# Kernel tuning notes

Measured on AMD Instinct MI355X. Metric: run time of the kernel, lower is better.

## Reference

```python
import jax, jax.numpy as jnp
import numpy as np
import math

N_HEADS = 16
D_HEAD = 128
D_ROPE = 32
SPLIT = D_HEAD - D_ROPE  # 96
LATENT = 512
D_MODEL = 2048
B, T = 2, 2048


def _rotary_emb(num_tokens, d_rope):
    inv_freq = 1.0 / (10000.0 ** (jnp.arange(0, d_rope, 2, dtype=jnp.float32) / d_rope))
    t = jnp.arange(num_tokens, dtype=jnp.float32)
    freqs = jnp.einsum('t,f->tf', t, inv_freq)          # [T, d_rope/2]
    return jnp.concatenate([freqs, freqs], axis=-1)      # [T, d_rope]


def _apply_rotary(x, cos, sin):
    # x: [B,T,H,d_rope]; cos/sin: [1,T,1,d_rope]
    half = x.shape[-1] // 2
    x1, x2 = x[..., :half], x[..., half:]
    rot = jnp.concatenate([-x2, x1], axis=-1)
    return x * cos + rot * sin


def setup_inputs() -> dict:
    key = jax.random.key(0)
    ks = jax.random.split(key, 20)
    s = 0.02
    def w(k, i, o):
        return jax.random.normal(k, (i, o), dtype=jnp.float32) * s
    inp = {
        'input': jax.random.normal(ks[0], (B, T, D_MODEL), dtype=jnp.float32),
        'batch_size': B,
        'num_tokens': T,
        'Wdkv_w': w(ks[1], D_MODEL, LATENT), 'Wdkv_b': jnp.zeros((LATENT,), jnp.float32),
        'Wdq_w':  w(ks[2], D_MODEL, LATENT), 'Wdq_b':  jnp.zeros((LATENT,), jnp.float32),
        'Wuk_w':  w(ks[3], LATENT, N_HEADS * SPLIT),  'Wuk_b': jnp.zeros((N_HEADS * SPLIT,), jnp.float32),
        'Wuv_w':  w(ks[4], LATENT, N_HEADS * D_HEAD), 'Wuv_b': jnp.zeros((N_HEADS * D_HEAD,), jnp.float32),
        'Wuq_w':  w(ks[5], LATENT, N_HEADS * SPLIT),  'Wuq_b': jnp.zeros((N_HEADS * SPLIT,), jnp.float32),
        'Wqr_w':  w(ks[6], LATENT, N_HEADS * D_ROPE), 'Wqr_b': jnp.zeros((N_HEADS * D_ROPE,), jnp.float32),
        'Wkr_w':  w(ks[7], D_MODEL, N_HEADS * D_ROPE), 'Wkr_b': jnp.zeros((N_HEADS * D_ROPE,), jnp.float32),
        'Wo_w':   w(ks[8], N_HEADS * D_HEAD, D_MODEL), 'Wo_b': jnp.zeros((D_MODEL,), jnp.float32),
    }
    return inp


def reference(input, batch_size, num_tokens,
              Wdkv_w, Wdkv_b, Wdq_w, Wdq_b, Wuk_w, Wuk_b, Wuv_w, Wuv_b,
              Wuq_w, Wuq_b, Wqr_w, Wqr_b, Wkr_w, Wkr_b, Wo_w, Wo_b):
    lin = lambda x, w, b: x @ w + b
    bsz, T_ = batch_size, num_tokens

    c_kv = lin(input, Wdkv_w, Wdkv_b)                                   # [B,T,latent]
    k_base = lin(c_kv, Wuk_w, Wuk_b).reshape(bsz, T_, N_HEADS, SPLIT)
    v = lin(c_kv, Wuv_w, Wuv_b).reshape(bsz, T_, N_HEADS, D_HEAD)

    c_q = lin(input, Wdq_w, Wdq_b)
    q_base = lin(c_q, Wuq_w, Wuq_b).reshape(bsz, T_, N_HEADS, SPLIT)
    q_rot = lin(c_q, Wqr_w, Wqr_b).reshape(bsz, T_, N_HEADS, D_ROPE)

    emb = _rotary_emb(T_, D_ROPE)                                        # [T,d_rope]
    cos = jnp.cos(emb)[None, :, None, :]
    sin = jnp.sin(emb)[None, :, None, :]
    q_rot = _apply_rotary(q_rot, cos, sin)
    k_rot = _apply_rotary(lin(input, Wkr_w, Wkr_b).reshape(bsz, T_, N_HEADS, D_ROPE), cos, sin)

    q = jnp.concatenate([q_base, q_rot], axis=-1)                        # [B,T,H,d_head]
    k = jnp.concatenate([k_base, k_rot], axis=-1)

    scores = jnp.einsum('bqhd,bkhd->bhqk', q, k) / math.sqrt(D_HEAD)
    attn = jax.nn.softmax(scores, axis=-1)
    out = jnp.einsum('bhqk,bkhd->bqhd', attn, v)
    out = lin(out.reshape(bsz, T_, N_HEADS * D_HEAD), Wo_w, Wo_b)
    return out, c_kv, k_rot
```

## Files before the change

kernel.cpp:

```cpp
#include <hip/hip_runtime.h>

typedef __bf16 bf16x8 __attribute__((ext_vector_type(8)));
typedef float f32x4 __attribute__((ext_vector_type(4)));
typedef float f32x16 __attribute__((ext_vector_type(16)));

#define NROWS 4096
#define DM 2048
#define LAT 512
#define NH 16
#define DH 128

__device__ __forceinline__ unsigned short f2bf(float f) {
    union { float f; unsigned u; } v; v.f = f;
    unsigned r = v.u + 0x7fffu + ((v.u >> 16) & 1u);
    return (unsigned short)(r >> 16);
}
__device__ __forceinline__ void gload16(const void* g, void* l) {
    __builtin_amdgcn_global_load_lds((const __attribute__((address_space(1))) unsigned int*)g,
                                     (__attribute__((address_space(3))) unsigned int*)l, 16, 0, 0);
}
__device__ __forceinline__ unsigned cvtpk_bf16(float lo, float hi) {
    unsigned r;
    asm("v_cvt_pk_bf16_f32 %0, %1, %2" : "=v"(r) : "v"(lo), "v"(hi));
    return r;
}
__device__ __forceinline__ void pl32swap(unsigned& a, unsigned& b) {
    asm("v_permlane32_swap_b32 %0, %1" : "+v"(a), "+v"(b));
}
__device__ __forceinline__ float exp2a(float x) {
    float r;
    asm("v_exp_f32 %0, %1" : "=v"(r) : "v"(x));
    return r;
}

struct PrepParams {
    const float* tsrc[8]; unsigned short* tdst[8];
    int tK[8]; int tN[8]; int tstart[8];
    const float* input; unsigned short* xbf;
    float* cs; float* sn;
    const float* bsrc[8]; float* bdst[8]; int blen[8];
};

#define PREP_T_END   9984
#define PREP_X_END   18176
#define PREP_R_END   18304
#define PREP_B_END   18340

__global__ __launch_bounds__(256) void prep_kernel(PrepParams P) {
    const int bid = blockIdx.x, tid = threadIdx.x;
    if (bid < PREP_T_END) {
        int j = 0;
        #pragma unroll
        for (int i = 1; i < 8; ++i) if (bid >= P.tstart[i]) j = i;
        const int local = bid - P.tstart[j];
        const float* W = P.tsrc[j];
        unsigned short* Wt = P.tdst[j];
        const int K = P.tK[j], N = P.tN[j];
        const int nbx = N >> 5;
        const int nb = (local % nbx) * 32, kb = (local / nbx) * 32;
        __shared__ float tile[32][33];
        const int tx = tid & 31, ty = tid >> 5;
        #pragma unroll
        for (int i = 0; i < 32; i += 8)
            tile[ty + i][tx] = W[(size_t)(kb + ty + i) * N + nb + tx];
        __syncthreads();
        #pragma unroll
        for (int i = 0; i < 32; i += 8)
            Wt[(size_t)(nb + ty + i) * K + kb + tx] = f2bf(tile[tx][ty + i]);
    } else if (bid < PREP_X_END) {
        const int i = ((bid - PREP_T_END) * 256 + tid) * 4;
        float4 v = *(const float4*)(P.input + i);
        unsigned short* y = P.xbf + i;
        y[0] = f2bf(v.x); y[1] = f2bf(v.y); y[2] = f2bf(v.z); y[3] = f2bf(v.w);
    } else if (bid < PREP_R_END) {
        const int idx = (bid - PREP_X_END) * 256 + tid;
        const int i = idx & 15, t = idx >> 4;
        float inv = powf(10000.0f, -(float)i / 16.0f);
        float a = (float)t * inv;
        P.cs[idx] = cosf(a);
        P.sn[idx] = sinf(a);
    } else {
        const int gid = (bid - PREP_R_END) * 256 + tid;
        int off = 0;
        #pragma unroll
        for (int i = 0; i < 8; ++i) {
            if (gid >= off && gid < off + P.blen[i])
                P.bdst[i][gid - off] = P.bsrc[i][gid - off];
            off += P.blen[i];
        }
    }
}

__global__ __launch_bounds__(256) void gemm_fused_kernel(const unsigned short* __restrict__ A,
                                                         const unsigned short* __restrict__ Bt,
                                                         const float* __restrict__ biascat,
                                                         int K, int which,
                                                         float* __restrict__ outF,
                                                         unsigned short* __restrict__ outB0,
                                                         unsigned short* __restrict__ outB1,
                                                         unsigned short* __restrict__ outB0k,
                                                         float* __restrict__ outRope,
                                                         const float* __restrict__ cs,
                                                         const float* __restrict__ sn) {
    __shared__ __align__(16) unsigned short SM[2][8192];
    const int tid = threadIdx.x;
    const int mb = blockIdx.x * 128;
    const int by = blockIdx.y, nb = by * 128;
    const int w = tid >> 6, lane = tid & 63;
    const int wr = (w >> 1) * 64, wc = (w & 1) * 64;
    const int l15 = lane & 15, l4 = lane >> 4;
    const int srow = lane >> 2, sko = (lane & 3) * 8;

    f32x4 acc[4][4] = {};

    auto STAGE = [&](int buf, int k0) {
        #pragma unroll
        for (int c = 0; c < 16; c += 4) {
            int cc = c + w;
            if (cc < 8)
                gload16(A + (size_t)(mb + cc * 16 + srow) * K + k0 + sko, SM[buf] + cc * 512);
            else
                gload16(Bt + (size_t)(nb + (cc - 8) * 16 + srow) * K + k0 + sko, SM[buf] + 4096 + (cc - 8) * 512);
        }
    };

    const int nk = K >> 5;
    STAGE(0, 0);
    for (int kt = 0; kt < nk; ++kt) {
        const int buf = kt & 1;
        if (kt + 1 < nk) {
            STAGE(buf ^ 1, (kt + 1) << 5);
            asm volatile("s_waitcnt vmcnt(4)" ::: "memory");
        } else {
            asm volatile("s_waitcnt vmcnt(0)" ::: "memory");
        }
        __builtin_amdgcn_sched_barrier(0);
        __builtin_amdgcn_s_barrier();
        __builtin_amdgcn_sched_barrier(0);

        const unsigned short* As = SM[buf];
        const unsigned short* Bs = SM[buf] + 4096;
        bf16x8 af[4], bfr[4];
        #pragma unroll
        for (int mi = 0; mi < 4; ++mi)
            af[mi] = *(const bf16x8*)(As + (wr + mi * 16 + l15) * 32 + l4 * 8);
        #pragma unroll
        for (int ni = 0; ni < 4; ++ni)
            bfr[ni] = *(const bf16x8*)(Bs + (wc + ni * 16 + l15) * 32 + l4 * 8);
        #pragma unroll
        for (int mi = 0; mi < 4; ++mi)
            #pragma unroll
            for (int ni = 0; ni < 4; ++ni)
                acc[mi][ni] = __builtin_amdgcn_mfma_f32_16x16x32_bf16(af[mi], bfr[ni], acc[mi][ni], 0, 0, 0);
        __builtin_amdgcn_s_barrier();
    }

    if (which == 1 && by >= 12) {
        unsigned short* BT = &SM[0][0];
        const int c2b = nb - 1536;
        #pragma unroll
        for (int half = 0; half < 2; ++half) {
            __syncthreads();
            if ((wr >> 6) == half) {
                #pragma unroll
                for (int mi = 0; mi < 4; ++mi)
                    #pragma unroll
                    for (int ni = 0; ni < 4; ++ni) {
                        const int col = wc + ni * 16 + l15;
                        const float bv = biascat[nb + col];
                        ushort4 pv;
                        pv.x = f2bf(acc[mi][ni][0] + bv);
                        pv.y = f2bf(acc[mi][ni][1] + bv);
                        pv.z = f2bf(acc[mi][ni][2] + bv);
                        pv.w = f2bf(acc[mi][ni][3] + bv);
                        *(ushort4*)(BT + col * 72 + mi * 16 + l4 * 4) = pv;
                    }
            }
            __syncthreads();
            const int c = tid >> 1;
            #pragma unroll
            for (int j = 0; j < 4; ++j) {
                const int seg = (tid & 1) * 4 + j;
                uint4 val = *(const uint4*)(BT + c * 72 + seg * 8);
                *(uint4*)(outB1 + (size_t)(c2b + c) * 4096 + mb + half * 64 + seg * 8) = val;
            }
        }
        return;
    }

    #pragma unroll
    for (int mi = 0; mi < 4; ++mi) {
        const int row0 = mb + wr + mi * 16 + l4 * 4;
        #pragma unroll
        for (int ni = 0; ni < 4; ++ni) {
            const int colg = nb + wc + ni * 16 + l15;
            const float bv = biascat[colg];
            float v[4];
            #pragma unroll
            for (int r = 0; r < 4; ++r) v[r] = acc[mi][ni][r] + bv;

            if (which == 0) {
                if (by < 4) {
                    #pragma unroll
                    for (int r = 0; r < 4; ++r) {
                        outF[(size_t)(row0 + r) * 512 + colg] = v[r];
                        outB0[(size_t)(row0 + r) * 512 + colg] = f2bf(v[r]);
                    }
                } else if (by < 8) {
                    const int c2 = colg - 512;
                    #pragma unroll
                    for (int r = 0; r < 4; ++r)
                        outB1[(size_t)(row0 + r) * 512 + c2] = f2bf(v[r]);
                } else {
                    const int cloc = colg - 1024, i2 = cloc & 31, h2 = cloc >> 5;
                    const float pbv = biascat[colg ^ 16];
                    const bool lo = (ni & 1) == 0;
                    #pragma unroll
                    for (int r = 0; r < 4; ++r) {
                        float vp = acc[mi][ni ^ 1][r] + pbv;
                        int t = (row0 + r) & 2047;
                        float cc_ = cs[t * 16 + (i2 & 15)], ss_ = sn[t * 16 + (i2 & 15)];
                        float o = lo ? (v[r] * cc_ - vp * ss_) : (v[r] * cc_ + vp * ss_);
                        outRope[(size_t)(row0 + r) * 512 + cloc] = o;
                        outB0k[(size_t)(row0 + r) * 2048 + h2 * 128 + 96 + i2] = f2bf(o);
                    }
                }
            } else if (which == 1) {
                const int ocol = (colg / 96) * 128 + colg % 96;
                #pragma unroll
                for (int r = 0; r < 4; ++r)
                    outB0[(size_t)(row0 + r) * 2048 + ocol] = f2bf(v[r]);
            } else if (which == 2) {
                if (by < 12) {
                    const int ocol = (colg / 96) * 128 + colg % 96;
                    #pragma unroll
                    for (int r = 0; r < 4; ++r)
                        outB0[(size_t)(row0 + r) * 2048 + ocol] = f2bf(v[r]);
                } else {
                    const int cloc = colg - 1536, i2 = cloc & 31, h2 = cloc >> 5;
                    const float pbv = biascat[colg ^ 16];
                    const bool lo = (ni & 1) == 0;
                    #pragma unroll
                    for (int r = 0; r < 4; ++r) {
                        float vp = acc[mi][ni ^ 1][r] + pbv;
                        int t = (row0 + r) & 2047;
                        float cc_ = cs[t * 16 + (i2 & 15)], ss_ = sn[t * 16 + (i2 & 15)];
                        float o = lo ? (v[r] * cc_ - vp * ss_) : (v[r] * cc_ + vp * ss_);
                        outB0[(size_t)(row0 + r) * 2048 + h2 * 128 + 96 + i2] = f2bf(o);
                    }
                }
            } else {
                #pragma unroll
                for (int r = 0; r < 4; ++r)
                    outF[(size_t)(row0 + r) * 2048 + colg] = v[r];
            }
        }
    }
}

__global__ __launch_bounds__(256, 2) void attn_kernel(const unsigned short* __restrict__ Q,
                                                      const unsigned short* __restrict__ Kb,
                                                      const unsigned short* __restrict__ Vtg,
                                                      unsigned short* __restrict__ O) {
    __shared__ __align__(16) unsigned short Ks[2][64 * 128];
    __shared__ __align__(16) unsigned short Vs[2][128 * 64];

    const int tid = threadIdx.x, w = tid >> 6, lane = tid & 63;
    const int l31 = lane & 31, hi = lane >> 5;
    const int bid = blockIdx.x;
    const int logical = (bid & 7) * 64 + (bid >> 3);
    const int bh = logical >> 4, b = bh >> 4, h = bh & 15;
    const int qt = (logical & 15) * 128 + w * 32;
    const int qrow = qt + l31;
    const float sl2e = 0.08838834764831845f * 1.4426950408889634f;

    bf16x8 qf[8];
    const unsigned short* qptr = Q + (size_t)(b * 2048 + qrow) * 2048 + h * 128 + hi * 8;
    #pragma unroll
    for (int s = 0; s < 8; ++s) qf[s] = *(const bf16x8*)(qptr + s * 16);

    f32x16 acc[4] = {};
    float m_run = -1e30f, l_run = 0.0f;

    const int kl15 = lane >> 4, kd0 = lane & 15;
    const int vr = lane >> 3, vk = lane & 7;

    auto STAGE = [&](int buf, int kt) {
        #pragma unroll
        for (int i = 0; i < 4; ++i) {
            int c = w * 4 + i;
            int key = c * 4 + kl15;
            int d0 = (kd0 * 8) ^ ((key & 7) << 3);
            gload16(Kb + (size_t)(b * 2048 + kt + key) * 2048 + h * 128 + d0, &Ks[buf][c * 512]);
            int dv = c * 8 + vr;
            int k0 = (vk * 8) ^ ((dv & 7) << 3);
            gload16(Vtg + (size_t)(h * 128 + dv) * 4096 + b * 2048 + kt + k0, &Vs[buf][c * 512]);
        }
    };

    STAGE(0, 0);

    for (int t = 0; t < 32; ++t) {
        const int buf = t & 1;
        if (t < 31) {
            STAGE(buf ^ 1, (t + 1) * 64);
            asm volatile("s_waitcnt vmcnt(8)" ::: "memory");
        } else {
            asm volatile("s_waitcnt vmcnt(0)" ::: "memory");
        }
        __builtin_amdgcn_sched_barrier(0);
        __builtin_amdgcn_s_barrier();
        __builtin_amdgcn_sched_barrier(0);

        #pragma unroll
        for (int g = 0; g < 2; ++g) {
            const int key = g * 32 + l31;
            const unsigned short* kbase = &Ks[buf][key * 128];
            const int ksw = (key & 7) << 3;
            f32x16 sc = {};
            __builtin_amdgcn_s_setprio(1);
            #pragma unroll
            for (int s = 0; s < 8; ++s) {
                bf16x8 kf = *(const bf16x8*)(kbase + ((s * 16 + hi * 8) ^ ksw));
                sc = __builtin_amdgcn_mfma_f32_32x32x16_bf16(kf, qf[s], sc, 0, 0, 0);
            }
            __builtin_amdgcn_s_setprio(0);

            float pm = sc[0];
            #pragma unroll
            for (int i = 1; i < 16; ++i) pm = fmaxf(pm, sc[i]);
            pm = fmaxf(pm, __shfl_xor(pm, 32, 64));

            if (__any(pm > m_run + 90.51f)) {
                float mn = fmaxf(m_run, pm);
                float f = exp2a((m_run - mn) * sl2e);
                m_run = mn;
                l_run *= f;
                #pragma unroll
                for (int dg = 0; dg < 4; ++dg)
                    #pragma unroll
                    for (int i = 0; i < 16; ++i) acc[dg][i] *= f;
            }
            const float mexp2 = m_run * sl2e;

            float rs = 0.0f;
            #pragma unroll
            for (int s2 = 0; s2 < 2; ++s2) {
                float e[8];
                #pragma unroll
                for (int j = 0; j < 8; ++j) {
                    e[j] = exp2a(fmaf(sc[s2 * 8 + j], sl2e, -mexp2));
                    rs += e[j];
                }
                unsigned X0 = cvtpk_bf16(e[0], e[1]), X1 = cvtpk_bf16(e[2], e[3]);
                unsigned Y0 = cvtpk_bf16(e[4], e[5]), Y1 = cvtpk_bf16(e[6], e[7]);
                pl32swap(X0, Y0);
                pl32swap(X1, Y1);
                union { unsigned u[4]; bf16x8 v; } pf;
                pf.u[0] = X0; pf.u[1] = X1; pf.u[2] = Y0; pf.u[3] = Y1;

                const int kofs = g * 32 + s2 * 16 + hi * 8;
                __builtin_amdgcn_s_setprio(1);
                #pragma unroll
                for (int dg = 0; dg < 4; ++dg) {
                    const int d = dg * 32 + l31;
                    bf16x8 vf = *(const bf16x8*)(&Vs[buf][d * 64 + (kofs ^ ((d & 7) << 3))]);
                    acc[dg] = __builtin_amdgcn_mfma_f32_32x32x16_bf16(vf, pf.v, acc[dg], 0, 0, 0);
                }
                __builtin_amdgcn_s_setprio(0);
            }
            rs += __shfl_xor(rs, 32, 64);
            l_run += rs;
        }
        __builtin_amdgcn_s_barrier();
    }

    const float inv = 1.0f / l_run;
    unsigned short* obase = O + (size_t)(b * 2048 + qrow) * 2048 + h * 128;
    #pragma unroll
    for (int dg = 0; dg < 4; ++dg)
        #pragma unroll
        for (int k = 0; k < 4; ++k) {
            ushort4 pv;
            pv.x = f2bf(acc[dg][4 * k + 0] * inv);
            pv.y = f2bf(acc[dg][4 * k + 1] * inv);
            pv.z = f2bf(acc[dg][4 * k + 2] * inv);
            pv.w = f2bf(acc[dg][4 * k + 3] * inv);
            *(ushort4*)(obase + dg * 32 + k * 8 + hi * 4) = pv;
        }
}

extern "C" void kernel_launch(void* const* d_in, const int* in_sizes, int n_in,
                              void* d_out, int out_size, void* d_ws, size_t ws_size,
                              hipStream_t stream) {
    (void)in_sizes; (void)n_in; (void)out_size; (void)ws_size;

    const float* input  = (const float*)d_in[0];
    const float* Wdkv_w = (const float*)d_in[3];
    const float* Wdkv_b = (const float*)d_in[4];
    const float* Wdq_w  = (const float*)d_in[5];
    const float* Wdq_b  = (const float*)d_in[6];
    const float* Wuk_w  = (const float*)d_in[7];
    const float* Wuk_b  = (const float*)d_in[8];
    const float* Wuv_w  = (const float*)d_in[9];
    const float* Wuv_b  = (const float*)d_in[10];
    const float* Wuq_w  = (const float*)d_in[11];
    const float* Wuq_b  = (const float*)d_in[12];
    const float* Wqr_w  = (const float*)d_in[13];
    const float* Wqr_b  = (const float*)d_in[14];
    const float* Wkr_w  = (const float*)d_in[15];
    const float* Wkr_b  = (const float*)d_in[16];
    const float* Wo_w   = (const float*)d_in[17];
    const float* Wo_b   = (const float*)d_in[18];

    float* out_main = (float*)d_out;
    float* out_ckv  = out_main + (size_t)NROWS * DM;
    float* out_krot = out_ckv + (size_t)NROWS * LAT;

    char* p = (char*)d_ws;
    auto alloc = [&](size_t bytes) { char* r = p; p += (bytes + 255) & ~(size_t)255; return r; };
    unsigned short* x_bf  = (unsigned short*)alloc((size_t)NROWS * DM * 2);
    unsigned short* w1_t  = (unsigned short*)alloc((size_t)1536 * DM * 2);
    unsigned short* w2_t  = (unsigned short*)alloc((size_t)3584 * LAT * 2);
    unsigned short* w3_t  = (unsigned short*)alloc((size_t)2048 * LAT * 2);
    unsigned short* w4_t  = (unsigned short*)alloc((size_t)DM * DM * 2);
    unsigned short* ckv_bf = (unsigned short*)alloc((size_t)NROWS * LAT * 2);
    unsigned short* cq_bf  = (unsigned short*)alloc((size_t)NROWS * LAT * 2);
    unsigned short* q_bf   = (unsigned short*)alloc((size_t)NROWS * DM * 2);
    unsigned short* k_bf   = (unsigned short*)alloc((size_t)NROWS * DM * 2);
    unsigned short* vt_g   = (unsigned short*)alloc((size_t)DM * NROWS * 2);
    unsigned short* ao_bf  = (unsigned short*)alloc((size_t)NROWS * DM * 2);
    float* cos_t = (float*)alloc((size_t)2048 * 16 * 4);
    float* sin_t = (float*)alloc((size_t)2048 * 16 * 4);
    float* bc1 = (float*)alloc(1536 * 4);
    float* bc2 = (float*)alloc(3584 * 4);
    float* bc3 = (float*)alloc(2048 * 4);
    float* bc4 = (float*)alloc(2048 * 4);

    PrepParams P;
    const float* tsrc[8] = {Wdkv_w, Wdq_w, Wkr_w, Wuk_w, Wuv_w, Wuq_w, Wqr_w, Wo_w};
    unsigned short* tdst[8] = {w1_t, w1_t + 512 * 2048, w1_t + 1024 * 2048,
                               w2_t, w2_t + 1536 * 512, w3_t, w3_t + 1536 * 512, w4_t};
    int tK[8] = {2048, 2048, 2048, 512, 512, 512, 512, 2048};
    int tN[8] = {512, 512, 512, 1536, 2048, 1536, 512, 2048};
    int tstart[8] = {0, 1024, 2048, 3072, 3840, 4864, 5632, 5888};
    const float* bsrc[8] = {Wdkv_b, Wdq_b, Wkr_b, Wuk_b, Wuv_b, Wuq_b, Wqr_b, Wo_b};
    float* bdst[8] = {bc1, bc1 + 512, bc1 + 1024, bc2, bc2 + 1536, bc3, bc3 + 1536, bc4};
    int blen[8] = {512, 512, 512, 1536, 2048, 1536, 512, 2048};
    for (int i = 0; i < 8; ++i) {
        P.tsrc[i] = tsrc[i]; P.tdst[i] = tdst[i]; P.tK[i] = tK[i]; P.tN[i] = tN[i];
        P.tstart[i] = tstart[i]; P.bsrc[i] = bsrc[i]; P.bdst[i] = bdst[i]; P.blen[i] = blen[i];
    }
    P.input = input; P.xbf = x_bf; P.cs = cos_t; P.sn = sin_t;
    prep_kernel<<<PREP_B_END, 256, 0, stream>>>(P);

    gemm_fused_kernel<<<dim3(32, 12), 256, 0, stream>>>(x_bf, w1_t, bc1, 2048, 0,
                                                        out_ckv, ckv_bf, cq_bf, k_bf, out_krot, cos_t, sin_t);
    gemm_fused_kernel<<<dim3(32, 28), 256, 0, stream>>>(ckv_bf, w2_t, bc2, 512, 1,
                                                        nullptr, k_bf, vt_g, nullptr, nullptr, nullptr, nullptr);
    gemm_fused_kernel<<<dim3(32, 16), 256, 0, stream>>>(cq_bf, w3_t, bc3, 512, 2,
                                                        nullptr, q_bf, nullptr, nullptr, nullptr, cos_t, sin_t);

    attn_kernel<<<512, 256, 0, stream>>>(q_bf, k_bf, vt_g, ao_bf);

    gemm_fused_kernel<<<dim3(32, 16), 256, 0, stream>>>(ao_bf, w4_t, bc4, 2048, 3,
                                                        out_main, nullptr, nullptr, nullptr, nullptr, nullptr, nullptr);
}
```

Before: 239.0 us.

## Split attention over two key halves with merge kernel and single-buffered V

Splits each attention block's key range into two halves, so the grid doubles to 1024 blocks. Each block writes unnormalized bf16 partial outputs plus running max and sum, and a new merge kernel combines them. V staging drops to a single buffer that loads while QK/softmax runs, QK MFMAs are split into two independent accumulator chains, and launch bounds rise to 3 blocks per CU. This targets low occupancy and serialized MFMA dependencies in the original 512-block launch. In exchange it adds partial-output traffic, an extra launch, and extra rounding from storing unnormalized partials in bf16.

```diff
diff --git a/kernel.cpp b/kernel.cpp
--- a/kernel.cpp
+++ b/kernel.cpp
@@ -258,20 +258,23 @@
     }
 }
 
-__global__ __launch_bounds__(256, 2) void attn_kernel(const unsigned short* __restrict__ Q,
+__global__ __launch_bounds__(256, 3) void attn_kernel(const unsigned short* __restrict__ Q,
                                                       const unsigned short* __restrict__ Kb,
                                                       const unsigned short* __restrict__ Vtg,
-                                                      unsigned short* __restrict__ O) {
+                                                      unsigned short* __restrict__ p0,
+                                                      unsigned short* __restrict__ p1,
+                                                      float* __restrict__ pml) {
     __shared__ __align__(16) unsigned short Ks[2][64 * 128];
-    __shared__ __align__(16) unsigned short Vs[2][128 * 64];
+    __shared__ __align__(16) unsigned short Vs[128 * 64];
 
     const int tid = threadIdx.x, w = tid >> 6, lane = tid & 63;
     const int l31 = lane & 31, hi = lane >> 5;
     const int bid = blockIdx.x;
-    const int logical = (bid & 7) * 64 + (bid >> 3);
-    const int bh = logical >> 4, b = bh >> 4, h = bh & 15;
-    const int qt = (logical & 15) * 128 + w * 32;
-    const int qrow = qt + l31;
+    const int logical = (bid & 7) * 128 + (bid >> 3);
+    const int bh = logical >> 5, b = bh >> 4, h = bh & 15;
+    const int ks = (logical >> 4) & 1;
+    const int qrow = (logical & 15) * 128 + w * 32 + l31;
+    const int kbase = ks * 1024;
     const float sl2e = 0.08838834764831845f * 1.4426950408889634f;
 
     bf16x8 qf[8];
@@ -285,50 +288,60 @@
     const int kl15 = lane >> 4, kd0 = lane & 15;
     const int vr = lane >> 3, vk = lane & 7;
 
-    auto STAGE = [&](int buf, int kt) {
+    auto STAGE_K = [&](int buf, int kt) {
         #pragma unroll
         for (int i = 0; i < 4; ++i) {
             int c = w * 4 + i;
             int key = c * 4 + kl15;
             int d0 = (kd0 * 8) ^ ((key & 7) << 3);
             gload16(Kb + (size_t)(b * 2048 + kt + key) * 2048 + h * 128 + d0, &Ks[buf][c * 512]);
+        }
+    };
+    auto STAGE_V = [&](int kt) {
+        #pragma unroll
+        for (int i = 0; i < 4; ++i) {
+            int c = w * 4 + i;
             int dv = c * 8 + vr;
             int k0 = (vk * 8) ^ ((dv & 7) << 3);
-            gload16(Vtg + (size_t)(h * 128 + dv) * 4096 + b * 2048 + kt + k0, &Vs[buf][c * 512]);
+            gload16(Vtg + (size_t)(h * 128 + dv) * 4096 + b * 2048 + kt + k0, &Vs[c * 512]);
         }
     };
 
-    STAGE(0, 0);
-
-    for (int t = 0; t < 32; ++t) {
+    STAGE_K(0, kbase);
+    asm volatile("s_waitcnt vmcnt(0)" ::: "memory");
+    __builtin_amdgcn_sched_barrier(0);
+    __builtin_amdgcn_s_barrier();
+    __builtin_amdgcn_sched_barrier(0);
+
+    for (int t = 0; t < 16; ++t) {
         const int buf = t & 1;
-        if (t < 31) {
-            STAGE(buf ^ 1, (t + 1) * 64);
-            asm volatile("s_waitcnt vmcnt(8)" ::: "memory");
-        } else {
-            asm volatile("s_waitcnt vmcnt(0)" ::: "memory");
-        }
-        __builtin_amdgcn_sched_barrier(0);
-        __builtin_amdgcn_s_barrier();
-        __builtin_amdgcn_sched_barrier(0);
-
+        STAGE_V(kbase + t * 64);
+        if (t < 15) STAGE_K(buf ^ 1, kbase + (t + 1) * 64);
+
+        unsigned pfu[2][2][4];
         #pragma unroll
         for (int g = 0; g < 2; ++g) {
             const int key = g * 32 + l31;
-            const unsigned short* kbase = &Ks[buf][key * 128];
+            const unsigned short* kbse = &Ks[buf][key * 128];
             const int ksw = (key & 7) << 3;
-            f32x16 sc = {};
+            f32x16 scA = {}, scB = {};
             __builtin_amdgcn_s_setprio(1);
             #pragma unroll
-            for (int s = 0; s < 8; ++s) {
-                bf16x8 kf = *(const bf16x8*)(kbase + ((s * 16 + hi * 8) ^ ksw));
-                sc = __builtin_amdgcn_mfma_f32_32x32x16_bf16(kf, qf[s], sc, 0, 0, 0);
+            for (int s = 0; s < 4; ++s) {
+                bf16x8 kfA = *(const bf16x8*)(kbse + ((s * 16 + hi * 8) ^ ksw));
+                bf16x8 kfB = *(const bf16x8*)(kbse + (((s + 4) * 16 + hi * 8) ^ ksw));
+                scA = __builtin_amdgcn_mfma_f32_32x32x16_bf16(kfA, qf[s], scA, 0, 0, 0);
+                scB = __builtin_amdgcn_mfma_f32_32x32x16_bf16(kfB, qf[s + 4], scB, 0, 0, 0);
             }
             __builtin_amdgcn_s_setprio(0);
-
-            float pm = sc[0];
-            #pragma unroll
-            for (int i = 1; i < 16; ++i) pm = fmaxf(pm, sc[i]);
+            f32x16 sc = scA + scB;
+
+            float t0 = fmaxf(sc[0], sc[1]),  t1 = fmaxf(sc[2], sc[3]);
+            float t2 = fmaxf(sc[4], sc[5]),  t3 = fmaxf(sc[6], sc[7]);
+            float t4 = fmaxf(sc[8], sc[9]),  t5 = fmaxf(sc[10], sc[11]);
+            float t6 = fmaxf(sc[12], sc[13]), t7 = fmaxf(sc[14], sc[15]);
+            float pm = fmaxf(fmaxf(fmaxf(t0, t1), fmaxf(t2, t3)),
+                             fmaxf(fmaxf(t4, t5), fmaxf(t6, t7)));
             pm = fmaxf(pm, __shfl_xor(pm, 32, 64));
 
             if (__any(pm > m_run + 90.51f)) {
@@ -343,51 +356,107 @@
             }
             const float mexp2 = m_run * sl2e;
 
-            float rs = 0.0f;
+            float e[16];
+            #pragma unroll
+            for (int j = 0; j < 16; ++j)
+                e[j] = exp2a(fmaf(sc[j], sl2e, -mexp2));
+            float a0 = e[0] + e[1], a1 = e[2] + e[3], a2 = e[4] + e[5], a3 = e[6] + e[7];
+            float a4 = e[8] + e[9], a5 = e[10] + e[11], a6 = e[12] + e[13], a7 = e[14] + e[15];
+            l_run += ((a0 + a1) + (a2 + a3)) + ((a4 + a5) + (a6 + a7));
+
             #pragma unroll
             for (int s2 = 0; s2 < 2; ++s2) {
-                float e[8];
-                #pragma unroll
-                for (int j = 0; j < 8; ++j) {
-                    e[j] = exp2a(fmaf(sc[s2 * 8 + j], sl2e, -mexp2));
-                    rs += e[j];
-                }
-                unsigned X0 = cvtpk_bf16(e[0], e[1]), X1 = cvtpk_bf16(e[2], e[3]);
-                unsigned Y0 = cvtpk_bf16(e[4], e[5]), Y1 = cvtpk_bf16(e[6], e[7]);
+                unsigned X0 = cvtpk_bf16(e[s2 * 8 + 0], e[s2 * 8 + 1]);
+                unsigned X1 = cvtpk_bf16(e[s2 * 8 + 2], e[s2 * 8 + 3]);
+                unsigned Y0 = cvtpk_bf16(e[s2 * 8 + 4], e[s2 * 8 + 5]);
+                unsigned Y1 = cvtpk_bf16(e[s2 * 8 + 6], e[s2 * 8 + 7]);
                 pl32swap(X0, Y0);
                 pl32swap(X1, Y1);
+                pfu[g][s2][0] = X0; pfu[g][s2][1] = X1;
+                pfu[g][s2][2] = Y0; pfu[g][s2][3] = Y1;
+            }
+        }
+
+        if (t < 15) asm volatile("s_waitcnt vmcnt(4)" ::: "memory");
+        else        asm volatile("s_waitcnt vmcnt(0)" ::: "memory");
+        __builtin_amdgcn_sched_barrier(0);
+        __builtin_amdgcn_s_barrier();
+        __builtin_amdgcn_sched_barrier(0);
+
+        __builtin_amdgcn_s_setprio(1);
+        #pragma unroll
+        for (int g = 0; g < 2; ++g)
+            #pragma unroll
+            for (int s2 = 0; s2 < 2; ++s2) {
                 union { unsigned u[4]; bf16x8 v; } pf;
-                pf.u[0] = X0; pf.u[1] = X1; pf.u[2] = Y0; pf.u[3] = Y1;
-
+                pf.u[0] = pfu[g][s2][0]; pf.u[1] = pfu[g][s2][1];
+                pf.u[2] = pfu[g][s2][2]; pf.u[3] = pfu[g][s2][3];
                 const int kofs = g * 32 + s2 * 16 + hi * 8;
-                __builtin_amdgcn_s_setprio(1);
                 #pragma unroll
                 for (int dg = 0; dg < 4; ++dg) {
                     const int d = dg * 32 + l31;
-                    bf16x8 vf = *(const bf16x8*)(&Vs[buf][d * 64 + (kofs ^ ((d & 7) << 3))]);
+                    bf16x8 vf = *(const bf16x8*)(&Vs[d * 64 + (kofs ^ ((d & 7) << 3))]);
                     acc[dg] = __builtin_amdgcn_mfma_f32_32x32x16_bf16(vf, pf.v, acc[dg], 0, 0, 0);
                 }
-                __builtin_amdgcn_s_setprio(0);
-            }
-            rs += __shfl_xor(rs, 32, 64);
-            l_run += rs;
-        }
-        __builtin_amdgcn_s_barrier();
-    }
-
-    const float inv = 1.0f / l_run;
-    unsigned short* obase = O + (size_t)(b * 2048 + qrow) * 2048 + h * 128;
+            }
+        __builtin_amdgcn_s_setprio(0);
+
+        if (t < 15) {
+            asm volatile("s_waitcnt vmcnt(0)" ::: "memory");
+            __builtin_amdgcn_sched_barrier(0);
+            __builtin_amdgcn_s_barrier();
+            __builtin_amdgcn_sched_barrier(0);
+        }
+    }
+
+    l_run += __shfl_xor(l_run, 32, 64);
+    unsigned short* pOut = (ks ? p1 : p0) + (size_t)(bh * 2048 + qrow) * 128;
+    if (hi == 0) {
+        float2 ml; ml.x = m_run; ml.y = l_run;
+        *(float2*)(pml + ((size_t)(ks * 32 + bh) * 2048 + qrow) * 2) = ml;
+    }
     #pragma unroll
     for (int dg = 0; dg < 4; ++dg)
         #pragma unroll
         for (int k = 0; k < 4; ++k) {
             ushort4 pv;
-            pv.x = f2bf(acc[dg][4 * k + 0] * inv);
-            pv.y = f2bf(acc[dg][4 * k + 1] * inv);
-            pv.z = f2bf(acc[dg][4 * k + 2] * inv);
-            pv.w = f2bf(acc[dg][4 * k + 3] * inv);
-            *(ushort4*)(obase + dg * 32 + k * 8 + hi * 4) = pv;
-        }
+            pv.x = f2bf(acc[dg][4 * k + 0]);
+            pv.y = f2bf(acc[dg][4 * k + 1]);
+            pv.z = f2bf(acc[dg][4 * k + 2]);
+            pv.w = f2bf(acc[dg][4 * k + 3]);
+            *(ushort4*)(pOut + dg * 32 + k * 8 + hi * 4) = pv;
+        }
+}
+
+__global__ __launch_bounds__(256) void attn_merge_kernel(const unsigned short* __restrict__ p0,
+                                                         const unsigned short* __restrict__ p1,
+                                                         const float* __restrict__ pml,
+                                                         unsigned short* __restrict__ O) {
+    const int idx = blockIdx.x * 256 + threadIdx.x;
+    const int d8 = idx & 15, t = (idx >> 4) & 2047, bh = idx >> 15;
+    const int b = bh >> 4, h = bh & 15;
+    const float sl2e = 0.08838834764831845f * 1.4426950408889634f;
+    const size_t base = (size_t)(bh * 2048 + t) * 128 + d8 * 8;
+    bf16x8 a = *(const bf16x8*)(p0 + base);
+    bf16x8 c = *(const bf16x8*)(p1 + base);
+    float2 ml0 = *(const float2*)(pml + ((size_t)(0 * 32 + bh) * 2048 + t) * 2);
+    float2 ml1 = *(const float2*)(pml + ((size_t)(1 * 32 + bh) * 2048 + t) * 2);
+    float M = fmaxf(ml0.x, ml1.x);
+    float w0 = exp2a((ml0.x - M) * sl2e);
+    float w1 = exp2a((ml1.x - M) * sl2e);
+    float inv = 1.0f / (w0 * ml0.y + w1 * ml1.y);
+    unsigned short* ob = O + (size_t)(b * 2048 + t) * 2048 + h * 128 + d8 * 8;
+    ushort4 o0, o1;
+    o0.x = f2bf((w0 * (float)a[0] + w1 * (float)c[0]) * inv);
+    o0.y = f2bf((w0 * (float)a[1] + w1 * (float)c[1]) * inv);
+    o0.z = f2bf((w0 * (float)a[2] + w1 * (float)c[2]) * inv);
+    o0.w = f2bf((w0 * (float)a[3] + w1 * (float)c[3]) * inv);
+    o1.x = f2bf((w0 * (float)a[4] + w1 * (float)c[4]) * inv);
+    o1.y = f2bf((w0 * (float)a[5] + w1 * (float)c[5]) * inv);
+    o1.z = f2bf((w0 * (float)a[6] + w1 * (float)c[6]) * inv);
+    o1.w = f2bf((w0 * (float)a[7] + w1 * (float)c[7]) * inv);
+    *(ushort4*)ob = o0;
+    *(ushort4*)(ob + 4) = o1;
 }
 
 extern "C" void kernel_launch(void* const* d_in, const int* in_sizes, int n_in,
@@ -430,6 +499,9 @@
     unsigned short* k_bf   = (unsigned short*)alloc((size_t)NROWS * DM * 2);
     unsigned short* vt_g   = (unsigned short*)alloc((size_t)DM * NROWS * 2);
     unsigned short* ao_bf  = (unsigned short*)alloc((size_t)NROWS * DM * 2);
+    unsigned short* part0  = (unsigned short*)alloc((size_t)NROWS * DM * 2);
+    unsigned short* part1  = (unsigned short*)alloc((size_t)NROWS * DM * 2);
+    float* pml  = (float*)alloc((size_t)2 * 32 * 2048 * 2 * 4);
     float* cos_t = (float*)alloc((size_t)2048 * 16 * 4);
     float* sin_t = (float*)alloc((size_t)2048 * 16 * 4);
     float* bc1 = (float*)alloc(1536 * 4);
@@ -461,7 +533,8 @@
     gemm_fused_kernel<<<dim3(32, 16), 256, 0, stream>>>(cq_bf, w3_t, bc3, 512, 2,
                                                         nullptr, q_bf, nullptr, nullptr, nullptr, cos_t, sin_t);
 
-    attn_kernel<<<512, 256, 0, stream>>>(q_bf, k_bf, vt_g, ao_bf);
+    attn_kernel<<<1024, 256, 0, stream>>>(q_bf, k_bf, vt_g, part0, part1, pml);
+    attn_merge_kernel<<<4096, 256, 0, stream>>>(part0, part1, pml, ao_bf);
 
     gemm_fused_kernel<<<dim3(32, 16), 256, 0, stream>>>(ao_bf, w4_t, bc4, 2048, 3,
                                                         out_main, nullptr, nullptr, nullptr, nullptr, nullptr, nullptr);
```

Result: slower. 296.8 us (+24.2%).
